# Kernel tuning notes

Hardware: AMD Instinct MI355X
Metric: run time of the kernel (lower is better)

Reference implementation:

```python
import jax, jax.numpy as jnp
import numpy as np

# DeepSeek-V3 MLA attention (q_lora_rank > 0 path), sdpa attn_type (causal)
B, S, DIM = 2, 2048, 2048
NH = 16
Q_LORA = 1536
KV_LORA = 512
NOPE = 128
ROPE = 64
VH = 128
QK_HD = NOPE + ROPE  # 192
EPS = 1e-6
SCALE = QK_HD ** -0.5
ROPE_THETA = 10000.0


def _freqs(seqlen, dim, base):
    f = 1.0 / base ** (np.arange(0, dim, 2, dtype=np.float32) / dim)
    ang = np.outer(np.arange(seqlen, dtype=np.float32), f)
    return jnp.asarray(np.cos(ang)), jnp.asarray(np.sin(ang))


def rmsnorm(x, w, eps=EPS):
    var = jnp.mean(jnp.square(x), axis=-1, keepdims=True)
    return x * jax.lax.rsqrt(var + eps) * w


def apply_rope(x, cos, sin):
    # x: [b, s, h, d]; cos/sin: [s, d//2]; interleaved complex pairs (x[2i], x[2i+1])
    xr, xi = x[..., 0::2], x[..., 1::2]
    c = cos[None, :, None, :]
    s = sin[None, :, None, :]
    yr = xr * c - xi * s
    yi = xr * s + xi * c
    return jnp.stack([yr, yi], axis=-1).reshape(x.shape)


def setup_inputs() -> dict:
    key = jax.random.key(0)
    ks = jax.random.split(key, 7)
    std = 0.02
    x = jax.random.normal(ks[0], (B, S, DIM), dtype=jnp.float32)
    cos, sin = _freqs(S, ROPE, ROPE_THETA)
    return {
        "x": x,
        "freqs_cos": cos,
        "freqs_sin": sin,
        "wq_a": jax.random.normal(ks[1], (DIM, Q_LORA), dtype=jnp.float32) * std,
        "q_norm_w": jnp.ones((Q_LORA,), dtype=jnp.float32),
        "wq_b": jax.random.normal(ks[2], (Q_LORA, NH * QK_HD), dtype=jnp.float32) * std,
        "wkv_a": jax.random.normal(ks[3], (DIM, KV_LORA + ROPE), dtype=jnp.float32) * std,
        "kv_norm_w": jnp.ones((KV_LORA,), dtype=jnp.float32),
        "wkv_b": jax.random.normal(ks[4], (KV_LORA, NH * (NOPE + VH)), dtype=jnp.float32) * std,
        "wo": jax.random.normal(ks[5], (NH * VH, DIM), dtype=jnp.float32) * std,
    }


def reference(x, freqs_cos, freqs_sin, wq_a, q_norm_w, wq_b, wkv_a, kv_norm_w, wkv_b, wo):
    b, s, _ = x.shape
    # low-rank Q projection: wq_a -> RMSNorm -> wq_b
    q = rmsnorm(x @ wq_a, q_norm_w) @ wq_b
    q = q.reshape(b, s, NH, QK_HD)
    q_nope, q_pe = q[..., :NOPE], q[..., NOPE:]
    q_pe = apply_rope(q_pe, freqs_cos, freqs_sin)
    q = jnp.concatenate([q_nope, q_pe], axis=-1)
    # low-rank KV: wkv_a -> split latent / rope part
    kv = x @ wkv_a
    kv_lat, k_pe = kv[..., :KV_LORA], kv[..., KV_LORA:]
    k_pe = apply_rope(k_pe[:, :, None, :], freqs_cos, freqs_sin)  # [b,s,1,ROPE]
    kv = rmsnorm(kv_lat, kv_norm_w) @ wkv_b
    kv = kv.reshape(b, s, NH, NOPE + VH)
    k_nope, v = kv[..., :NOPE], kv[..., NOPE:]
    k = jnp.concatenate([k_nope, jnp.broadcast_to(k_pe, (b, s, NH, ROPE))], axis=-1)
    # attention [b,h,s,d]
    q = q.transpose(0, 2, 1, 3)
    k = k.transpose(0, 2, 1, 3)
    v = v.transpose(0, 2, 1, 3)
    scores = jnp.einsum("bhqd,bhkd->bhqk", q, k) * SCALE
    causal = jnp.tril(jnp.ones((s, s), dtype=bool))
    scores = jnp.where(causal[None, None], scores, jnp.finfo(scores.dtype).min)
    probs = jax.nn.softmax(scores, axis=-1)
    out = jnp.einsum("bhqk,bhkd->bhqd", probs, v)
    out = out.transpose(0, 2, 1, 3).reshape(b, s, NH * VH)
    return out @ wo
```

## Files before the change

### kernel.cpp

```cpp
#include <hip/hip_runtime.h>
#include <cstdint>
#include <cstddef>

typedef __attribute__((ext_vector_type(8))) short bf16x8;
typedef __attribute__((ext_vector_type(4))) float f32x4;
typedef __attribute__((ext_vector_type(16))) float f32x16;

#define S_LEN 2048
#define SCALE2 0.10411754f

__device__ __forceinline__ ushort f2bf(float f) {
  uint32_t u = __float_as_uint(f);
  u = (u + 0x7FFFu + ((u >> 16) & 1u)) >> 16;
  return (ushort)u;
}
__device__ __forceinline__ float bf2f(ushort u) {
  return __uint_as_float(((uint32_t)u) << 16);
}

typedef __attribute__((address_space(1))) void GV;
typedef __attribute__((address_space(3))) void LV;
__device__ __forceinline__ void gload16(const void* g, void* l) {
  __builtin_amdgcn_global_load_lds((GV*)g, (LV*)l, 16, 0, 0);
}

__device__ __forceinline__ void store_out(float* p, float v) { *p = v; }
__device__ __forceinline__ void store_out(ushort* p, float v) { *p = f2bf(v); }

__global__ void k_f32_to_bf16(const float* __restrict__ in, ushort* __restrict__ out, int n4) {
  int i = blockIdx.x * blockDim.x + threadIdx.x;
  int stride = gridDim.x * blockDim.x;
  for (; i < n4; i += stride) {
    float4 v = reinterpret_cast<const float4*>(in)[i];
    ushort4 o;
    o.x = f2bf(v.x); o.y = f2bf(v.y); o.z = f2bf(v.z); o.w = f2bf(v.w);
    reinterpret_cast<ushort4*>(out)[i] = o;
  }
}

__global__ void k_transpose_f32_bf16(const float* __restrict__ in, ushort* __restrict__ out,
                                     int R, int C) {
  __shared__ float tile[32][33];
  int c0 = blockIdx.x * 32, r0 = blockIdx.y * 32;
  int tx = threadIdx.x, ty = threadIdx.y;
#pragma unroll
  for (int i = 0; i < 32; i += 8) {
    int r = r0 + ty + i, c = c0 + tx;
    if (r < R && c < C) tile[ty + i][tx] = in[(size_t)r * C + c];
  }
  __syncthreads();
#pragma unroll
  for (int i = 0; i < 32; i += 8) {
    int c = c0 + ty + i, r = r0 + tx;
    if (r < R && c < C) out[(size_t)c * R + r] = f2bf(tile[tx][ty + i]);
  }
}

template <typename OUT>
__global__ __launch_bounds__(256) void k_gemm(const ushort* __restrict__ A,
                                              const ushort* __restrict__ Bt,
                                              OUT* __restrict__ C, int K, int Nreal) {
  __shared__ ushort As[128 * 32];
  __shared__ ushort Bs[128 * 32];
  const int t = threadIdx.x, lane = t & 63, w = t >> 6;
  const int nwg = gridDim.x * gridDim.y;
  const int wg = blockIdx.y * gridDim.x + blockIdx.x;
  const int swz = (wg & 7) * (nwg >> 3) + (wg >> 3);
  const int m0 = (swz / gridDim.x) * 128, n0 = (swz % gridDim.x) * 128;
  const int wm = (w >> 1) * 64, wn = (w & 1) * 64;
  const int g = lane >> 4, q = lane & 15;
  f32x4 acc[4][4] = {};
  for (int kt = 0; kt < K; kt += 32) {
#pragma unroll
    for (int i = 0; i < 2; i++) {
      int idx = i * 256 + t;
      gload16(A + (size_t)(m0 + (idx >> 2)) * K + kt + (idx & 3) * 8,
              (char*)As + (size_t)(i * 256 + (w << 6)) * 16);
      gload16(Bt + (size_t)(n0 + (idx >> 2)) * K + kt + (idx & 3) * 8,
              (char*)Bs + (size_t)(i * 256 + (w << 6)) * 16);
    }
    __syncthreads();
    bf16x8 af[4], bfr[4];
#pragma unroll
    for (int mi = 0; mi < 4; mi++) af[mi] = *(const bf16x8*)(As + (wm + 16 * mi + q) * 32 + 8 * g);
#pragma unroll
    for (int ni = 0; ni < 4; ni++) bfr[ni] = *(const bf16x8*)(Bs + (wn + 16 * ni + q) * 32 + 8 * g);
#pragma unroll
    for (int mi = 0; mi < 4; mi++)
#pragma unroll
      for (int ni = 0; ni < 4; ni++)
        acc[mi][ni] = __builtin_amdgcn_mfma_f32_16x16x32_bf16(af[mi], bfr[ni], acc[mi][ni], 0, 0, 0);
    __syncthreads();
  }
#pragma unroll
  for (int mi = 0; mi < 4; mi++)
#pragma unroll
    for (int ni = 0; ni < 4; ni++) {
      int col = n0 + wn + 16 * ni + q;
      if (col < Nreal) {
        int row = m0 + wm + 16 * mi + 4 * g;
#pragma unroll
        for (int r = 0; r < 4; r++)
          store_out(&C[(size_t)(row + r) * Nreal + col], acc[mi][ni][r]);
      }
    }
}

__global__ __launch_bounds__(256) void k_gemm_kv(const ushort* __restrict__ A,
                                                 const ushort* __restrict__ Bt,
                                                 ushort* __restrict__ kbuf,
                                                 ushort* __restrict__ vT, int K) {
  __shared__ ushort As[128 * 32];
  __shared__ ushort Bs[128 * 32];
  const int t = threadIdx.x, lane = t & 63, w = t >> 6;
  const int nwg = gridDim.x * gridDim.y;
  const int wg = blockIdx.y * gridDim.x + blockIdx.x;
  const int swz = (wg & 7) * (nwg >> 3) + (wg >> 3);
  const int m0 = (swz / gridDim.x) * 128, n0 = (swz % gridDim.x) * 128;
  const int wm = (w >> 1) * 64, wn = (w & 1) * 64;
  const int g = lane >> 4, q = lane & 15;
  f32x4 acc[4][4] = {};
  for (int kt = 0; kt < K; kt += 32) {
#pragma unroll
    for (int i = 0; i < 2; i++) {
      int idx = i * 256 + t;
      gload16(A + (size_t)(m0 + (idx >> 2)) * K + kt + (idx & 3) * 8,
              (char*)As + (size_t)(i * 256 + (w << 6)) * 16);
      gload16(Bt + (size_t)(n0 + (idx >> 2)) * K + kt + (idx & 3) * 8,
              (char*)Bs + (size_t)(i * 256 + (w << 6)) * 16);
    }
    __syncthreads();
    bf16x8 af[4], bfr[4];
#pragma unroll
    for (int mi = 0; mi < 4; mi++) af[mi] = *(const bf16x8*)(As + (wm + 16 * mi + q) * 32 + 8 * g);
#pragma unroll
    for (int ni = 0; ni < 4; ni++) bfr[ni] = *(const bf16x8*)(Bs + (wn + 16 * ni + q) * 32 + 8 * g);
#pragma unroll
    for (int mi = 0; mi < 4; mi++)
#pragma unroll
      for (int ni = 0; ni < 4; ni++)
        acc[mi][ni] = __builtin_amdgcn_mfma_f32_16x16x32_bf16(af[mi], bfr[ni], acc[mi][ni], 0, 0, 0);
    __syncthreads();
  }
#pragma unroll
  for (int mi = 0; mi < 4; mi++)
#pragma unroll
    for (int ni = 0; ni < 4; ni++) {
      int col = n0 + wn + 16 * ni + q;
      int hh = col >> 8, jj = col & 255;
      int row0 = m0 + wm + 16 * mi + 4 * g;
#pragma unroll
      for (int r = 0; r < 4; r++) {
        int tok = row0 + r;
        int bb = tok >> 11, ss = tok & 2047;
        ushort v = f2bf(acc[mi][ni][r]);
        if (jj < 128)
          kbuf[((size_t)(bb * 16 + hh) * 2048 + ss) * 192 + jj] = v;
        else
          vT[((size_t)(bb * 16 + hh) * 128 + (jj - 128)) * 2048 + ss] = v;
      }
    }
}

__global__ void k_rmsnorm_bf16(const float* __restrict__ in, const float* __restrict__ w,
                               ushort* __restrict__ out, int D, int instride) {
  int row = blockIdx.x;
  const float* x = in + (size_t)row * instride;
  ushort* o = out + (size_t)row * D;
  float ss = 0.f;
  for (int i = threadIdx.x; i < D; i += 256) { float v = x[i]; ss += v * v; }
#pragma unroll
  for (int m = 1; m < 64; m <<= 1) ss += __shfl_xor(ss, m);
  __shared__ float red[4];
  if ((threadIdx.x & 63) == 0) red[threadIdx.x >> 6] = ss;
  __syncthreads();
  float tot = red[0] + red[1] + red[2] + red[3];
  float sc = rsqrtf(tot / (float)D + 1e-6f);
  for (int i = threadIdx.x; i < D; i += 256) o[i] = f2bf(x[i] * sc * w[i]);
}

__global__ void k_kvnorm_rope(const float* __restrict__ cqkv, const float* __restrict__ w,
                              const float* __restrict__ cosT, const float* __restrict__ sinT,
                              ushort* __restrict__ ckvn, ushort* __restrict__ kbuf) {
  int tok = blockIdx.x, b = tok >> 11, s = tok & 2047;
  const float* x = cqkv + (size_t)tok * 2112 + 1536;
  float ss = 0.f;
  for (int i = threadIdx.x; i < 512; i += 256) { float v = x[i]; ss += v * v; }
#pragma unroll
  for (int m = 1; m < 64; m <<= 1) ss += __shfl_xor(ss, m);
  __shared__ float red[4];
  if ((threadIdx.x & 63) == 0) red[threadIdx.x >> 6] = ss;
  __syncthreads();
  float tot = red[0] + red[1] + red[2] + red[3];
  float sc = rsqrtf(tot / 512.f + 1e-6f);
  for (int i = threadIdx.x; i < 512; i += 256) ckvn[(size_t)tok * 512 + i] = f2bf(x[i] * sc * w[i]);
  if (threadIdx.x < 32) {
    int i = threadIdx.x;
    float xr = x[512 + 2 * i], xi = x[512 + 2 * i + 1];
    float c = cosT[s * 32 + i], sn = sinT[s * 32 + i];
    uint32_t lo = f2bf(xr * c - xi * sn);
    uint32_t hi = f2bf(xr * sn + xi * c);
    uint32_t pk = lo | (hi << 16);
#pragma unroll
    for (int h = 0; h < 16; ++h)
      *(uint32_t*)(kbuf + ((size_t)(b * 16 + h) * 2048 + s) * 192 + 128 + 2 * i) = pk;
  }
}

__global__ void k_qrope(ushort* __restrict__ qb, const float* __restrict__ cosT,
                        const float* __restrict__ sinT) {
  int tok = blockIdx.x, s = tok & (S_LEN - 1);
  for (int pp = threadIdx.x; pp < 512; pp += 256) {
    int h = pp >> 5, i = pp & 31;
    ushort* base = qb + ((size_t)tok * 16 + h) * 192 + 128;
    float xr = bf2f(base[2 * i]), xi = bf2f(base[2 * i + 1]);
    float c = cosT[s * 32 + i], sn = sinT[s * 32 + i];
    base[2 * i] = f2bf(xr * c - xi * sn);
    base[2 * i + 1] = f2bf(xr * sn + xi * c);
  }
}

__global__ __launch_bounds__(256, 2) void k_attn10(const ushort* __restrict__ qb,
                                                   const ushort* __restrict__ kb,
                                                   const ushort* __restrict__ vT,
                                                   ushort* __restrict__ aout) {
  const int id = blockIdx.x;
  const int qt = 15 - (id >> 5);
  const int bh = id & 31;
  const int h = bh & 15, b = bh >> 4;

  const int t = threadIdx.x, lane = t & 63, w = t >> 6;
  const int lq = lane & 31, hi = lane >> 5;
  const int kx = (lq >> 3) & 3;

  __shared__ ushort Ks[64 * 200];
  __shared__ ushort Vs[128 * 72];

  const ushort* kh = kb + (size_t)(b * 16 + h) * (2048 * 192);
  const ushort* vh = vT + (size_t)(b * 16 + h) * (128 * 2048);

  auto stage = [&](int k0) {
#pragma unroll
    for (int it = 0; it < 7; ++it) {
      int ii = it * 4 + w;
      if (ii < 25) {
        unsigned s = ii * 64 + lane;
        int r = s / 25, e = s - r * 25;
        int cg = e ^ ((r >> 3) & 3);
        if (cg > 23) cg = 0;
        gload16(kh + (size_t)(k0 + r) * 192 + cg * 8, (char*)Ks + ii * 1024);
      }
    }
#pragma unroll
    for (int it = 0; it < 5; ++it) {
      int ii = it * 4 + w;
      if (ii < 18) {
        unsigned s = ii * 64 + lane;
        int r = s / 9, e = s - r * 9;
        int cg = e ^ ((r >> 3) & 7);
        if (cg > 7) cg = 0;
        gload16(vh + (size_t)r * 2048 + k0 + cg * 8, (char*)Vs + ii * 1024);
      }
    }
  };

  const int q0 = qt * 128;
  const int q0w = q0 + 32 * w;
  const int qg = q0w + lq;
  const int nkt = qt * 2 + 2;

  bf16x8 qf[12];
  {
    const ushort* qp = qb + ((size_t)(b * 2048 + qg) * 16 + h) * 192 + 8 * hi;
#pragma unroll
    for (int s = 0; s < 12; ++s) qf[s] = *(const bf16x8*)(qp + 16 * s);
  }

  f32x16 oacc[4];
#pragma unroll
  for (int db = 0; db < 4; ++db)
#pragma unroll
    for (int r = 0; r < 16; ++r) oacc[db][r] = 0.f;
  float m = -1e30f, l = 0.f;

  for (int kt = 0; kt < nkt; ++kt) {
    const int k0 = kt * 64;
    stage(k0);
    asm volatile("s_waitcnt vmcnt(0)" ::: "memory");
    __syncthreads();
    if (k0 <= q0w + 31) {
      f32x16 sA, sB;
#pragma unroll
      for (int r = 0; r < 16; ++r) { sA[r] = 0.f; sB[r] = 0.f; }
      __builtin_amdgcn_s_setprio(1);
#pragma unroll
      for (int s = 0; s < 12; ++s) {
        int ch = ((2 * s + hi) ^ kx) << 3;
        bf16x8 kfA = *(const bf16x8*)(Ks + lq * 200 + ch);
        bf16x8 kfB = *(const bf16x8*)(Ks + (lq + 32) * 200 + ch);
        sA = __builtin_amdgcn_mfma_f32_32x32x16_bf16(kfA, qf[s], sA, 0, 0, 0);
        sB = __builtin_amdgcn_mfma_f32_32x32x16_bf16(kfB, qf[s], sB, 0, 0, 0);
      }
      __builtin_amdgcn_s_setprio(0);
      float svA[16], svB[16];
#pragma unroll
      for (int r = 0; r < 16; ++r) { svA[r] = sA[r]; svB[r] = sB[r]; }
      if (k0 + 63 > q0w) {
#pragma unroll
        for (int r = 0; r < 16; ++r) {
          int kk = (r & 3) + 8 * (r >> 2) + 4 * hi;
          if (k0 + kk > qg) svA[r] = -1e30f;
          if (k0 + 32 + kk > qg) svB[r] = -1e30f;
        }
      }
      float pmax = fmaxf(svA[0], svB[0]);
#pragma unroll
      for (int r = 1; r < 16; ++r) pmax = fmaxf(pmax, fmaxf(svA[r], svB[r]));
      pmax = fmaxf(pmax, __shfl_xor(pmax, 32));
      float smax = pmax * SCALE2;
      if (!__all(smax - m <= 8.0f)) {
        float mnew = fmaxf(m, smax);
        float a = exp2f(m - mnew);
        l *= a;
#pragma unroll
        for (int db = 0; db < 4; ++db)
#pragma unroll
          for (int r = 0; r < 16; ++r) oacc[db][r] *= a;
        m = mnew;
      }
      float eA[16], eB[16]; float sum = 0.f;
#pragma unroll
      for (int r = 0; r < 16; ++r) {
        eA[r] = exp2f(svA[r] * SCALE2 - m);
        eB[r] = exp2f(svB[r] * SCALE2 - m);
        sum += eA[r] + eB[r];
      }
      sum += __shfl_xor(sum, 32);
      l += sum;
      uint32_t pkA[8], pkB[8];
#pragma unroll
      for (int i = 0; i < 8; ++i) {
        pkA[i] = (uint32_t)f2bf(eA[2 * i]) | ((uint32_t)f2bf(eA[2 * i + 1]) << 16);
        pkB[i] = (uint32_t)f2bf(eB[2 * i]) | ((uint32_t)f2bf(eB[2 * i + 1]) << 16);
      }
      uint32_t swA[8], swB[8];
#pragma unroll
      for (int i = 0; i < 8; ++i) {
        swA[i] = (uint32_t)__shfl_xor((int)pkA[i], 32);
        swB[i] = (uint32_t)__shfl_xor((int)pkB[i], 32);
      }
      union { uint32_t u[4]; bf16x8 v; } pA0, pA1, pB0, pB1;
      pA0.u[0] = hi ? swA[2] : pkA[0];
      pA0.u[1] = hi ? swA[3] : pkA[1];
      pA0.u[2] = hi ? pkA[2] : swA[0];
      pA0.u[3] = hi ? pkA[3] : swA[1];
      pA1.u[0] = hi ? swA[6] : pkA[4];
      pA1.u[1] = hi ? swA[7] : pkA[5];
      pA1.u[2] = hi ? pkA[6] : swA[4];
      pA1.u[3] = hi ? pkA[7] : swA[5];
      pB0.u[0] = hi ? swB[2] : pkB[0];
      pB0.u[1] = hi ? swB[3] : pkB[1];
      pB0.u[2] = hi ? pkB[2] : swB[0];
      pB0.u[3] = hi ? pkB[3] : swB[1];
      pB1.u[0] = hi ? swB[6] : pkB[4];
      pB1.u[1] = hi ? swB[7] : pkB[5];
      pB1.u[2] = hi ? pkB[6] : swB[4];
      pB1.u[3] = hi ? pkB[7] : swB[5];
      __builtin_amdgcn_s_setprio(1);
#pragma unroll
      for (int db = 0; db < 4; ++db) {
        const int d = 32 * db + lq;
        const int vx = (d >> 3) & 7;
        const ushort* vr = Vs + d * 72;
        bf16x8 vf0 = *(const bf16x8*)(vr + (((0 + hi) ^ vx) << 3));
        bf16x8 vf1 = *(const bf16x8*)(vr + (((2 + hi) ^ vx) << 3));
        bf16x8 vf2 = *(const bf16x8*)(vr + (((4 + hi) ^ vx) << 3));
        bf16x8 vf3 = *(const bf16x8*)(vr + (((6 + hi) ^ vx) << 3));
        oacc[db] = __builtin_amdgcn_mfma_f32_32x32x16_bf16(vf0, pA0.v, oacc[db], 0, 0, 0);
        oacc[db] = __builtin_amdgcn_mfma_f32_32x32x16_bf16(vf1, pA1.v, oacc[db], 0, 0, 0);
        oacc[db] = __builtin_amdgcn_mfma_f32_32x32x16_bf16(vf2, pB0.v, oacc[db], 0, 0, 0);
        oacc[db] = __builtin_amdgcn_mfma_f32_32x32x16_bf16(vf3, pB1.v, oacc[db], 0, 0, 0);
      }
      __builtin_amdgcn_s_setprio(0);
    }
    asm volatile("s_waitcnt lgkmcnt(0)" ::: "memory");
    __syncthreads();
  }

  float inv = 1.f / l;
  ushort* op = aout + ((size_t)(b * 2048 + qg)) * 2048 + h * 128 + 4 * hi;
#pragma unroll
  for (int db = 0; db < 4; ++db)
#pragma unroll
    for (int i = 0; i < 8; ++i) {
      uint32_t u = (uint32_t)f2bf(oacc[db][2 * i] * inv) |
                   ((uint32_t)f2bf(oacc[db][2 * i + 1] * inv) << 16);
      int dbase = 32 * db + (i & 1) * 2 + (i >> 1) * 8;
      *(uint32_t*)(op + dbase) = u;
    }
}

extern "C" void kernel_launch(void* const* d_in, const int* in_sizes, int n_in,
                              void* d_out, int out_size, void* d_ws, size_t ws_size,
                              hipStream_t stream) {
  const float* x = (const float*)d_in[0];
  const float* fcos = (const float*)d_in[1];
  const float* fsin = (const float*)d_in[2];
  const float* wq_a = (const float*)d_in[3];
  const float* qnw = (const float*)d_in[4];
  const float* wq_b = (const float*)d_in[5];
  const float* wkv_a = (const float*)d_in[6];
  const float* kvnw = (const float*)d_in[7];
  const float* wkv_b = (const float*)d_in[8];
  const float* wo = (const float*)d_in[9];
  float* out = (float*)d_out;

  char* ws = (char*)d_ws;
  size_t off = 0;
  auto alloc = [&](size_t bytes) -> char* {
    char* p = ws + off;
    off += (bytes + 255) & ~(size_t)255;
    return p;
  };
  ushort* xb     = (ushort*)alloc(4096ull * 2048 * 2);
  ushort* wqkv_t = (ushort*)alloc(2176ull * 2048 * 2);
  ushort* wqb_t  = (ushort*)alloc(3072ull * 1536 * 2);
  ushort* wkvb_t = (ushort*)alloc(4096ull * 512 * 2);
  ushort* wo_t   = (ushort*)alloc(2048ull * 2048 * 2);
  float*  cqkv   = (float*)alloc(4096ull * 2112 * 4);
  ushort* cqn    = (ushort*)alloc(4096ull * 1536 * 2);
  ushort* ckvn   = (ushort*)alloc(4096ull * 512 * 2);
  ushort* kbuf   = (ushort*)alloc(2ull * 16 * 2048 * 192 * 2);
  ushort* qbuf   = (ushort*)cqkv;
  ushort* aout   = xb;
  ushort* vT     = wqkv_t;

  dim3 tb(32, 8);
  k_f32_to_bf16<<<2048, 256, 0, stream>>>(x, xb, 4096 * 2048 / 4);
  k_transpose_f32_bf16<<<dim3(48, 64), tb, 0, stream>>>(wq_a, wqkv_t, 2048, 1536);
  k_transpose_f32_bf16<<<dim3(18, 64), tb, 0, stream>>>(wkv_a, wqkv_t + 1536ull * 2048, 2048, 576);
  k_transpose_f32_bf16<<<dim3(96, 48), tb, 0, stream>>>(wq_b, wqb_t, 1536, 3072);
  k_transpose_f32_bf16<<<dim3(128, 16), tb, 0, stream>>>(wkv_b, wkvb_t, 512, 4096);
  k_transpose_f32_bf16<<<dim3(64, 64), tb, 0, stream>>>(wo, wo_t, 2048, 2048);

  k_gemm<float><<<dim3(17, 32), 256, 0, stream>>>(xb, wqkv_t, cqkv, 2048, 2112);

  k_rmsnorm_bf16<<<4096, 256, 0, stream>>>(cqkv, qnw, cqn, 1536, 2112);
  k_kvnorm_rope<<<4096, 256, 0, stream>>>(cqkv, kvnw, fcos, fsin, ckvn, kbuf);

  k_gemm<ushort><<<dim3(24, 32), 256, 0, stream>>>(cqn, wqb_t, qbuf, 1536, 3072);
  k_qrope<<<4096, 256, 0, stream>>>(qbuf, fcos, fsin);

  k_gemm_kv<<<dim3(32, 32), 256, 0, stream>>>(ckvn, wkvb_t, kbuf, vT, 512);

  k_attn10<<<dim3(512), 256, 0, stream>>>(qbuf, kbuf, vT, aout);

  k_gemm<float><<<dim3(16, 32), 256, 0, stream>>>(aout, wo_t, out, 2048, 2048);
}
```

Measured before the change: 388.1 us.

## Double K-tile depth in GEMMs and use padded XOR-swizzled LDS layout

Both GEMM kernels now stage a 64-wide K slice per iteration instead of 32, halving the number of barrier/load rounds. The LDS rows are padded to 72 elements and the 8-element column groups are XOR-swizzled by row, so the MFMA fragment reads avoid bank conflicts; the direct-to-LDS loads are remapped to fill this layout, with the padding slot receiving a dummy load. The cost is more LDS per block, which may lower occupancy, plus extra index arithmetic (a divide by 9) in the load loop.

```diff
diff --git a/kernel.cpp b/kernel.cpp
--- a/kernel.cpp
+++ b/kernel.cpp
@@ -60,8 +60,8 @@
 __global__ __launch_bounds__(256) void k_gemm(const ushort* __restrict__ A,
                                               const ushort* __restrict__ Bt,
                                               OUT* __restrict__ C, int K, int Nreal) {
-  __shared__ ushort As[128 * 32];
-  __shared__ ushort Bs[128 * 32];
+  __shared__ ushort As[128 * 72];
+  __shared__ ushort Bs[128 * 72];
   const int t = threadIdx.x, lane = t & 63, w = t >> 6;
   const int nwg = gridDim.x * gridDim.y;
   const int wg = blockIdx.y * gridDim.x + blockIdx.x;
@@ -70,26 +70,42 @@
   const int wm = (w >> 1) * 64, wn = (w & 1) * 64;
   const int g = lane >> 4, q = lane & 15;
   f32x4 acc[4][4] = {};
-  for (int kt = 0; kt < K; kt += 32) {
-#pragma unroll
-    for (int i = 0; i < 2; i++) {
-      int idx = i * 256 + t;
-      gload16(A + (size_t)(m0 + (idx >> 2)) * K + kt + (idx & 3) * 8,
-              (char*)As + (size_t)(i * 256 + (w << 6)) * 16);
-      gload16(Bt + (size_t)(n0 + (idx >> 2)) * K + kt + (idx & 3) * 8,
-              (char*)Bs + (size_t)(i * 256 + (w << 6)) * 16);
-    }
-    __syncthreads();
-    bf16x8 af[4], bfr[4];
-#pragma unroll
-    for (int mi = 0; mi < 4; mi++) af[mi] = *(const bf16x8*)(As + (wm + 16 * mi + q) * 32 + 8 * g);
-#pragma unroll
-    for (int ni = 0; ni < 4; ni++) bfr[ni] = *(const bf16x8*)(Bs + (wn + 16 * ni + q) * 32 + 8 * g);
-#pragma unroll
-    for (int mi = 0; mi < 4; mi++)
-#pragma unroll
-      for (int ni = 0; ni < 4; ni++)
-        acc[mi][ni] = __builtin_amdgcn_mfma_f32_16x16x32_bf16(af[mi], bfr[ni], acc[mi][ni], 0, 0, 0);
+  for (int kt = 0; kt < K; kt += 64) {
+#pragma unroll
+    for (int it = 0; it < 5; ++it) {
+      int ii = it * 4 + w;
+      if (ii < 18) {
+        unsigned s = ii * 64 + lane;
+        int r = s / 9, e = s - r * 9;
+        int cg = e ^ ((r >> 3) & 7);
+        if (cg > 7) cg = 0;
+        gload16(A + (size_t)(m0 + r) * K + kt + cg * 8, (char*)As + ii * 1024);
+        gload16(Bt + (size_t)(n0 + r) * K + kt + cg * 8, (char*)Bs + ii * 1024);
+      }
+    }
+    asm volatile("s_waitcnt vmcnt(0)" ::: "memory");
+    __syncthreads();
+#pragma unroll
+    for (int kh = 0; kh < 2; ++kh) {
+      bf16x8 af[4], bfr[4];
+#pragma unroll
+      for (int mi = 0; mi < 4; mi++) {
+        int row = wm + 16 * mi + q;
+        int rx = (row >> 3) & 7;
+        af[mi] = *(const bf16x8*)(As + row * 72 + (((kh * 4 + g) ^ rx) << 3));
+      }
+#pragma unroll
+      for (int ni = 0; ni < 4; ni++) {
+        int row = wn + 16 * ni + q;
+        int rx = (row >> 3) & 7;
+        bfr[ni] = *(const bf16x8*)(Bs + row * 72 + (((kh * 4 + g) ^ rx) << 3));
+      }
+#pragma unroll
+      for (int mi = 0; mi < 4; mi++)
+#pragma unroll
+        for (int ni = 0; ni < 4; ni++)
+          acc[mi][ni] = __builtin_amdgcn_mfma_f32_16x16x32_bf16(af[mi], bfr[ni], acc[mi][ni], 0, 0, 0);
+    }
     __syncthreads();
   }
 #pragma unroll
@@ -110,8 +126,8 @@
                                                  const ushort* __restrict__ Bt,
                                                  ushort* __restrict__ kbuf,
                                                  ushort* __restrict__ vT, int K) {
-  __shared__ ushort As[128 * 32];
-  __shared__ ushort Bs[128 * 32];
+  __shared__ ushort As[128 * 72];
+  __shared__ ushort Bs[128 * 72];
   const int t = threadIdx.x, lane = t & 63, w = t >> 6;
   const int nwg = gridDim.x * gridDim.y;
   const int wg = blockIdx.y * gridDim.x + blockIdx.x;
@@ -120,26 +136,42 @@
   const int wm = (w >> 1) * 64, wn = (w & 1) * 64;
   const int g = lane >> 4, q = lane & 15;
   f32x4 acc[4][4] = {};
-  for (int kt = 0; kt < K; kt += 32) {
-#pragma unroll
-    for (int i = 0; i < 2; i++) {
-      int idx = i * 256 + t;
-      gload16(A + (size_t)(m0 + (idx >> 2)) * K + kt + (idx & 3) * 8,
-              (char*)As + (size_t)(i * 256 + (w << 6)) * 16);
-      gload16(Bt + (size_t)(n0 + (idx >> 2)) * K + kt + (idx & 3) * 8,
-              (char*)Bs + (size_t)(i * 256 + (w << 6)) * 16);
-    }
-    __syncthreads();
-    bf16x8 af[4], bfr[4];
-#pragma unroll
-    for (int mi = 0; mi < 4; mi++) af[mi] = *(const bf16x8*)(As + (wm + 16 * mi + q) * 32 + 8 * g);
-#pragma unroll
-    for (int ni = 0; ni < 4; ni++) bfr[ni] = *(const bf16x8*)(Bs + (wn + 16 * ni + q) * 32 + 8 * g);
-#pragma unroll
-    for (int mi = 0; mi < 4; mi++)
-#pragma unroll
-      for (int ni = 0; ni < 4; ni++)
-        acc[mi][ni] = __builtin_amdgcn_mfma_f32_16x16x32_bf16(af[mi], bfr[ni], acc[mi][ni], 0, 0, 0);
+  for (int kt = 0; kt < K; kt += 64) {
+#pragma unroll
+    for (int it = 0; it < 5; ++it) {
+      int ii = it * 4 + w;
+      if (ii < 18) {
+        unsigned s = ii * 64 + lane;
+        int r = s / 9, e = s - r * 9;
+        int cg = e ^ ((r >> 3) & 7);
+        if (cg > 7) cg = 0;
+        gload16(A + (size_t)(m0 + r) * K + kt + cg * 8, (char*)As + ii * 1024);
+        gload16(Bt + (size_t)(n0 + r) * K + kt + cg * 8, (char*)Bs + ii * 1024);
+      }
+    }
+    asm volatile("s_waitcnt vmcnt(0)" ::: "memory");
+    __syncthreads();
+#pragma unroll
+    for (int kh = 0; kh < 2; ++kh) {
+      bf16x8 af[4], bfr[4];
+#pragma unroll
+      for (int mi = 0; mi < 4; mi++) {
+        int row = wm + 16 * mi + q;
+        int rx = (row >> 3) & 7;
+        af[mi] = *(const bf16x8*)(As + row * 72 + (((kh * 4 + g) ^ rx) << 3));
+      }
+#pragma unroll
+      for (int ni = 0; ni < 4; ni++) {
+        int row = wn + 16 * ni + q;
+        int rx = (row >> 3) & 7;
+        bfr[ni] = *(const bf16x8*)(Bs + row * 72 + (((kh * 4 + g) ^ rx) << 3));
+      }
+#pragma unroll
+      for (int mi = 0; mi < 4; mi++)
+#pragma unroll
+        for (int ni = 0; ni < 4; ni++)
+          acc[mi][ni] = __builtin_amdgcn_mfma_f32_16x16x32_bf16(af[mi], bfr[ni], acc[mi][ni], 0, 0, 0);
+    }
     __syncthreads();
   }
 #pragma unroll
```

Result: faster. 354.8 us (-8.6%).
